# Kernel optimization log

Hardware: AMD Instinct MI355X
Metric: run time of the kernel (lower is better)

The kernel has to match this reference:

```python
import jax, jax.numpy as jnp
import numpy as np

NEG_SLOPE = 0.01  # torch.nn.LeakyReLU default


def setup_inputs() -> dict:
    key = jax.random.key(0)
    k1, k2, k3, k4, k5 = jax.random.split(key, 5)
    n_nodes, n_sources, d_in, d_out = 20000, 2048, 128, 128
    x = jax.random.normal(k1, (n_nodes, d_in), dtype=jnp.float32)
    A = jax.random.normal(k2, (n_nodes, n_sources), dtype=jnp.float32)
    W = jax.random.normal(k3, (d_in, d_in), dtype=jnp.float32) * (1.0 / np.sqrt(d_in))
    dense0_w = jax.random.normal(k4, (d_out, d_in), dtype=jnp.float32) * (1.0 / np.sqrt(d_in))
    src_idx = jnp.sort(jax.random.randint(k5, (n_sources,), 0, n_nodes, dtype=jnp.int64))
    return {"x": x, "A": A, "W": W, "dense0_w": dense0_w, "src_idx": src_idx}


def reference(x, A, W, dense0_w, src_idx):
    # GCNConv_Fixed_W: gather source nodes, shared weight transform, adjacency matmul
    support = x[src_idx] @ W                 # [n_sources, d_in]
    out = A @ support                        # [n_nodes, d_in]
    # nonlin + stacked Linear (1 layer, no bias)
    out = jnp.where(out >= 0, out, NEG_SLOPE * out)  # LeakyReLU
    out = out @ dense0_w.T                   # [n_nodes, d_out]
    return out
```

## Files before the change

### kernel.cpp

```cpp
#include <hip/hip_runtime.h>
#include <stdint.h>

#define NNODES 20000
#define NSRC   2048
#define DIN    128

typedef short s16x8 __attribute__((ext_vector_type(8)));
typedef unsigned short u16x8 __attribute__((ext_vector_type(8)));
typedef float f32x4 __attribute__((ext_vector_type(4)));

static __device__ __forceinline__ unsigned short f2bf(float f) {
  union { float f; unsigned int u; } v; v.f = f;
  unsigned int r = v.u + 0x7FFFu + ((v.u >> 16) & 1u);
  return (unsigned short)(r >> 16);
}

static __device__ __forceinline__ s16x8 pack8(float4 a, float4 b) {
  s16x8 r;
  r[0] = (short)f2bf(a.x); r[1] = (short)f2bf(a.y);
  r[2] = (short)f2bf(a.z); r[3] = (short)f2bf(a.w);
  r[4] = (short)f2bf(b.x); r[5] = (short)f2bf(b.y);
  r[6] = (short)f2bf(b.z); r[7] = (short)f2bf(b.w);
  return r;
}

static __device__ __forceinline__ s16x8 load_cvt8(const float* __restrict__ p) {
  return pack8(*reinterpret_cast<const float4*>(p),
               *reinterpret_cast<const float4*>(p + 4));
}

#define GLL16(g, l)                                                          \
  __builtin_amdgcn_global_load_lds(                                          \
      (const __attribute__((address_space(1))) void*)(g),                    \
      (__attribute__((address_space(3))) void*)(l), 16, 0, 0)

__global__ __launch_bounds__(128) void support_kernel(
    const float* __restrict__ x, const float* __restrict__ W,
    const int* __restrict__ src_idx, unsigned short* __restrict__ supTp) {
  __shared__ float xrows[8][DIN];
  const int j = threadIdx.x;
  const int s0 = blockIdx.x * 8;
#pragma unroll
  for (int i = 0; i < 8; ++i) {
    const int src = src_idx[s0 + i];
    xrows[i][j] = x[(size_t)src * DIN + j];
  }
  __syncthreads();
  float acc[8];
#pragma unroll
  for (int i = 0; i < 8; ++i) acc[i] = 0.f;
  for (int k = 0; k < DIN; ++k) {
    const float w = W[(size_t)k * DIN + j];
#pragma unroll
    for (int i = 0; i < 8; ++i) acc[i] += xrows[i][k] * w;
  }
  u16x8 o;
#pragma unroll
  for (int i = 0; i < 8; ++i) o[i] = f2bf(acc[i]);
  const int kk = s0 >> 5;
  const int g2 = (s0 >> 3) & 3;
  const int n = j >> 4;
  const int lane = (j & 15) + g2 * 16;
  *reinterpret_cast<u16x8*>(&supTp[(size_t)((kk * 8 + n) * 64 + lane) * 8]) = o;
}

__global__ __launch_bounds__(128) void fused_gcn_kernel(
    const float* __restrict__ A,
    const unsigned short* __restrict__ supTp,
    const float* __restrict__ Wd,
    float* __restrict__ out) {
  const int tid = threadIdx.x;
  const int lane = tid & 63;
  const int w = tid >> 6;
  const int r16 = lane & 15;
  const int g = lane >> 4;
  const int rowBase = blockIdx.x * 32;

  __shared__ __attribute__((aligned(16))) unsigned char pool[49152];
  float* Ap = (float*)pool;
  unsigned short* Bp = (unsigned short*)(pool + 16384);

  f32x4 acc[8];
#pragma unroll
  for (int n = 0; n < 8; ++n) acc[n] = (f32x4){0.f, 0.f, 0.f, 0.f};

#define STAGE(buf, c)                                                         \
  {                                                                           \
    _Pragma("unroll") for (int i2 = 0; i2 < 4; ++i2) {                        \
      const int i = w * 4 + i2;                                               \
      const int row = 4 * i + (lane >> 4);                                    \
      GLL16(A + (size_t)(rowBase + row) * NSRC + (c) * 64 +                   \
                (((lane & 15) ^ (row & 7)) << 2),                             \
            Ap + (buf) * 2048 + i * 256);                                     \
    }                                                                         \
    _Pragma("unroll") for (int i2 = 0; i2 < 8; ++i2) {                        \
      const int iB = w * 8 + i2;                                              \
      GLL16(supTp +                                                           \
                ((size_t)(((c) * 2 + (iB >> 3)) * 8 + (iB & 7)) * 64 + lane)  \
                    * 8,                                                      \
            Bp + (buf) * 8192 + iB * 512);                                    \
    }                                                                         \
  }

#define COMPUTE(buf)                                                          \
  {                                                                           \
    _Pragma("unroll") for (int kk2 = 0; kk2 < 2; ++kk2) {                     \
      const float* rb = Ap + (buf) * 2048 + (w * 16 + r16) * 64;              \
      const float4 lo = *reinterpret_cast<const float4*>(                     \
          &rb[((kk2 * 8 + g * 2) ^ (r16 & 7)) << 2]);                         \
      const float4 hi = *reinterpret_cast<const float4*>(                     \
          &rb[((kk2 * 8 + g * 2 + 1) ^ (r16 & 7)) << 2]);                     \
      const s16x8 a = pack8(lo, hi);                                          \
      _Pragma("unroll") for (int n = 0; n < 8; ++n) {                         \
        const s16x8 b = *reinterpret_cast<const s16x8*>(                      \
            &Bp[(buf) * 8192 + ((kk2 * 8 + n) * 64 + lane) * 8]);             \
        acc[n] =                                                              \
            __builtin_amdgcn_mfma_f32_16x16x32_bf16(a, b, acc[n], 0, 0, 0);   \
      }                                                                       \
    }                                                                         \
  }

  STAGE(0, 0);
  for (int c = 0; c < 31; ++c) {
    STAGE((c & 1) ^ 1, c + 1);
    asm volatile("s_waitcnt vmcnt(12)" ::: "memory");
    __builtin_amdgcn_s_barrier();
    COMPUTE(c & 1);
    __builtin_amdgcn_s_barrier();
  }
  asm volatile("s_waitcnt vmcnt(0)" ::: "memory");
  __builtin_amdgcn_s_barrier();
  COMPUTE(1);

  __builtin_amdgcn_s_barrier();
  unsigned short* actw = (unsigned short*)pool + w * 2176;
#pragma unroll
  for (int n = 0; n < 8; ++n)
#pragma unroll
    for (int r = 0; r < 4; ++r) {
      float v = acc[n][r];
      v = (v >= 0.f) ? v : 0.01f * v;
      actw[(g * 4 + r) * 136 + n * 16 + r16] = f2bf(v);
    }

  f32x4 acc2[8];
#pragma unroll
  for (int n = 0; n < 8; ++n) acc2[n] = (f32x4){0.f, 0.f, 0.f, 0.f};
#pragma unroll
  for (int k2 = 0; k2 < 4; ++k2) {
    const int k = k2 * 32 + g * 8;
    const s16x8 a2 = *reinterpret_cast<const s16x8*>(&actw[r16 * 136 + k]);
#pragma unroll
    for (int n = 0; n < 8; ++n) {
      const s16x8 b2 = load_cvt8(Wd + (size_t)(n * 16 + r16) * DIN + k);
      acc2[n] =
          __builtin_amdgcn_mfma_f32_16x16x32_bf16(a2, b2, acc2[n], 0, 0, 0);
    }
  }
#pragma unroll
  for (int n = 0; n < 8; ++n)
#pragma unroll
    for (int r = 0; r < 4; ++r)
      out[(size_t)(rowBase + w * 16 + g * 4 + r) * DIN + n * 16 + r16] =
          acc2[n][r];
}

extern "C" void kernel_launch(void* const* d_in, const int* in_sizes, int n_in,
                              void* d_out, int out_size, void* d_ws, size_t ws_size,
                              hipStream_t stream) {
  const float* x   = (const float*)d_in[0];
  const float* A   = (const float*)d_in[1];
  const float* W   = (const float*)d_in[2];
  const float* Wd  = (const float*)d_in[3];
  const int*   src = (const int*)d_in[4];
  float* out = (float*)d_out;

  unsigned short* supTp = (unsigned short*)d_ws;

  support_kernel<<<NSRC / 8, 128, 0, stream>>>(x, W, src, supTp);
  fused_gcn_kernel<<<NNODES / 32, 128, 0, stream>>>(A, supTp, Wd, out);
}
```

Baseline: 65.31 us.

## Stream support tiles from global into registers and drop block barriers

The support operand is no longer staged through LDS; each wave loads its B fragments directly from global memory (served from L2) into registers every chunk. Each wave now stages only its own 16 rows of A in a private double buffer, prefetching two chunks ahead, so both workgroup barriers in the main loop are removed. The LDS footprint shrinks from 48KB to about 20KB, which should allow more resident blocks to hide latency. In exchange, both waves fetch the same support data redundantly, and the L2 latency of the B loads sits on each iteration's critical path.

```diff
diff --git a/kernel.cpp b/kernel.cpp
--- a/kernel.cpp
+++ b/kernel.cpp
@@ -4,6 +4,7 @@
 #define NNODES 20000
 #define NSRC   2048
 #define DIN    128
+#define BM     32
 
 typedef short s16x8 __attribute__((ext_vector_type(8)));
 typedef unsigned short u16x8 __attribute__((ext_vector_type(8)));
@@ -74,66 +75,66 @@
   const int w = tid >> 6;
   const int r16 = lane & 15;
   const int g = lane >> 4;
-  const int rowBase = blockIdx.x * 32;
+  const int rowBase = blockIdx.x * BM;
 
-  __shared__ __attribute__((aligned(16))) unsigned char pool[49152];
-  float* Ap = (float*)pool;
-  unsigned short* Bp = (unsigned short*)(pool + 16384);
+  __shared__ float Ap[2][2][16 * 64];
+  __shared__ unsigned short act[2][16 * 136];
 
   f32x4 acc[8];
 #pragma unroll
   for (int n = 0; n < 8; ++n) acc[n] = (f32x4){0.f, 0.f, 0.f, 0.f};
 
-#define STAGE(buf, c)                                                         \
+#define ISSUE_A(buf, c)                                                       \
   {                                                                           \
     _Pragma("unroll") for (int i2 = 0; i2 < 4; ++i2) {                        \
-      const int i = w * 4 + i2;                                               \
-      const int row = 4 * i + (lane >> 4);                                    \
-      GLL16(A + (size_t)(rowBase + row) * NSRC + (c) * 64 +                   \
-                (((lane & 15) ^ (row & 7)) << 2),                             \
-            Ap + (buf) * 2048 + i * 256);                                     \
-    }                                                                         \
-    _Pragma("unroll") for (int i2 = 0; i2 < 8; ++i2) {                        \
-      const int iB = w * 8 + i2;                                              \
-      GLL16(supTp +                                                           \
-                ((size_t)(((c) * 2 + (iB >> 3)) * 8 + (iB & 7)) * 64 + lane)  \
-                    * 8,                                                      \
-            Bp + (buf) * 8192 + iB * 512);                                    \
+      const int rl = i2 * 4 + (lane >> 4);                                    \
+      GLL16(A + (size_t)(rowBase + w * 16 + rl) * NSRC + (c) * 64 +           \
+                (((lane & 15) ^ (rl & 7)) << 2),                              \
+            &Ap[w][buf][i2 * 256]);                                           \
     }                                                                         \
   }
 
-#define COMPUTE(buf)                                                          \
-  {                                                                           \
-    _Pragma("unroll") for (int kk2 = 0; kk2 < 2; ++kk2) {                     \
-      const float* rb = Ap + (buf) * 2048 + (w * 16 + r16) * 64;              \
-      const float4 lo = *reinterpret_cast<const float4*>(                     \
-          &rb[((kk2 * 8 + g * 2) ^ (r16 & 7)) << 2]);                         \
-      const float4 hi = *reinterpret_cast<const float4*>(                     \
-          &rb[((kk2 * 8 + g * 2 + 1) ^ (r16 & 7)) << 2]);                     \
-      const s16x8 a = pack8(lo, hi);                                          \
-      _Pragma("unroll") for (int n = 0; n < 8; ++n) {                         \
-        const s16x8 b = *reinterpret_cast<const s16x8*>(                      \
-            &Bp[(buf) * 8192 + ((kk2 * 8 + n) * 64 + lane) * 8]);             \
-        acc[n] =                                                              \
-            __builtin_amdgcn_mfma_f32_16x16x32_bf16(a, b, acc[n], 0, 0, 0);   \
-      }                                                                       \
-    }                                                                         \
+  ISSUE_A(0, 0);
+  ISSUE_A(1, 1);
+
+  for (int c = 0; c < 32; ++c) {
+    if (c < 31) {
+      asm volatile("s_waitcnt vmcnt(4)" ::: "memory");
+    } else {
+      asm volatile("s_waitcnt vmcnt(0)" ::: "memory");
+    }
+    const unsigned short* bsrc = supTp + (size_t)c * 8192;
+    s16x8 b0[8], b1[8];
+#pragma unroll
+    for (int n = 0; n < 8; ++n)
+      b0[n] = *reinterpret_cast<const s16x8*>(&bsrc[(size_t)(n * 64 + lane) * 8]);
+#pragma unroll
+    for (int n = 0; n < 8; ++n)
+      b1[n] = *reinterpret_cast<const s16x8*>(
+          &bsrc[(size_t)((8 + n) * 64 + lane) * 8]);
+    const float* rb = &Ap[w][c & 1][r16 * 64];
+    s16x8 afr[2];
+#pragma unroll
+    for (int kk2 = 0; kk2 < 2; ++kk2) {
+      const int t0 = kk2 * 8 + g * 2;
+      const float4 lo =
+          *reinterpret_cast<const float4*>(&rb[((t0) ^ (r16 & 7)) << 2]);
+      const float4 hi =
+          *reinterpret_cast<const float4*>(&rb[((t0 + 1) ^ (r16 & 7)) << 2]);
+      afr[kk2] = pack8(lo, hi);
+    }
+    asm volatile("s_waitcnt lgkmcnt(0)" ::: "memory");
+    __builtin_amdgcn_sched_barrier(0);
+    if (c < 30) ISSUE_A(c & 1, c + 2);
+#pragma unroll
+    for (int n = 0; n < 8; ++n)
+      acc[n] = __builtin_amdgcn_mfma_f32_16x16x32_bf16(afr[0], b0[n], acc[n], 0, 0, 0);
+#pragma unroll
+    for (int n = 0; n < 8; ++n)
+      acc[n] = __builtin_amdgcn_mfma_f32_16x16x32_bf16(afr[1], b1[n], acc[n], 0, 0, 0);
   }
 
-  STAGE(0, 0);
-  for (int c = 0; c < 31; ++c) {
-    STAGE((c & 1) ^ 1, c + 1);
-    asm volatile("s_waitcnt vmcnt(12)" ::: "memory");
-    __builtin_amdgcn_s_barrier();
-    COMPUTE(c & 1);
-    __builtin_amdgcn_s_barrier();
-  }
-  asm volatile("s_waitcnt vmcnt(0)" ::: "memory");
-  __builtin_amdgcn_s_barrier();
-  COMPUTE(1);
-
-  __builtin_amdgcn_s_barrier();
-  unsigned short* actw = (unsigned short*)pool + w * 2176;
+  unsigned short* actw = act[w];
 #pragma unroll
   for (int n = 0; n < 8; ++n)
 #pragma unroll
@@ -178,5 +179,5 @@
   unsigned short* supTp = (unsigned short*)d_ws;
 
   support_kernel<<<NSRC / 8, 128, 0, stream>>>(x, W, src, supTp);
-  fused_gcn_kernel<<<NNODES / 32, 128, 0, stream>>>(A, supTp, Wd, out);
+  fused_gcn_kernel<<<NNODES / BM, 128, 0, stream>>>(A, supTp, Wd, out);
 }
```

After: 70.74 us. 1.08x slower.
